# Kernel optimization log

Measured on AMD Instinct MI355X. Metric: run time of the kernel, lower is better.

The kernel has to match this reference:

```python
import jax, jax.numpy as jnp
import numpy as np

DF = 16
B, D, H, W = 2, 64, 64, 64


def _shift(a, axis, s):
    """Return a shifted so out[i] = a[i+s] along `axis`, zero-padded."""
    pad = [(0, 0)] * a.ndim
    pad[axis] = (1, 1)
    ap = jnp.pad(a, pad)
    idx = [slice(None)] * a.ndim
    idx[axis] = slice(1 + s, 1 + s + a.shape[axis])
    return ap[tuple(idx)]


def _image_grad(x, sum_axis):
    """Faithful replica of ImageGradient's (buggy) dense kernel.

    Uses only input channel 1; central difference along W; summed over the
    3 taps along `sum_axis` (1=D for pos==1, 2=H for pos==2); result is
    identical across all output channels.
    x: [B, C, D, H, W] -> [B, C, D, H, W]
    """
    s = x[:, 1]  # [B, D, H, W]
    g = 0.5 * (_shift(s, 3, 1) - _shift(s, 3, -1))  # d/dW central diff
    g3 = _shift(g, sum_axis, -1) + g + _shift(g, sum_axis, 1)
    return jnp.broadcast_to(g3[:, None], x.shape)


def _pconv(x, w, b):
    """nn.Conv3d(cin, cout, 1, padding=1): zero-pad spatial dims then 1x1x1 conv."""
    xp = jnp.pad(x, ((0, 0), (0, 0), (1, 1), (1, 1), (1, 1)))
    return jnp.einsum('bcdhw,oc->bodhw', xp, w) + b[None, :, None, None, None]


def setup_inputs() -> dict:
    key = jax.random.key(0)
    ks = jax.random.split(key, 8)
    p = jax.random.normal(ks[0], (B, DF, D, H, W), dtype=jnp.float32)
    q = jax.random.normal(ks[1], (B, DF, D, H, W), dtype=jnp.float32)
    W1 = jax.random.normal(ks[2], (DF, 6 * DF), dtype=jnp.float32) / np.sqrt(6 * DF)
    b1 = jax.random.normal(ks[3], (DF,), dtype=jnp.float32) * 0.01
    W2 = jax.random.normal(ks[4], (DF, DF), dtype=jnp.float32) / np.sqrt(DF)
    b2 = jax.random.normal(ks[5], (DF,), dtype=jnp.float32) * 0.01
    W3 = jax.random.normal(ks[6], (1, DF), dtype=jnp.float32) / np.sqrt(DF)
    b3 = jax.random.normal(ks[7], (1,), dtype=jnp.float32) * 0.01
    return {"p": p, "q": q, "W1": W1, "b1": b1, "W2": W2, "b2": b2, "W3": W3, "b3": b3}


def reference(p, q, W1, b1, W2, b2, W3, b3):
    dpx = _image_grad(p, 1)  # gradx: pos==1, sum over kd (D axis)
    dpy = _image_grad(p, 2)  # grady: pos==2, sum over kh (H axis)
    dqx = _image_grad(q, 1)
    dqy = _image_grad(q, 2)
    h = jnp.concatenate([p, dpx, dpy, q, dqx, dqy], axis=1)  # [B, 6*DF, D, H, W]
    h = jax.nn.relu(_pconv(h, W1, b1))  # [B, DF, D+2, H+2, W+2]
    h = jax.nn.relu(_pconv(h, W2, b2))  # [B, DF, D+4, H+4, W+4]
    h = jax.nn.relu(_pconv(h, W3, b3))  # [B, 1, D+6, H+6, W+6]
    return (h, p, dpx, dpy, q, dqx, dqy)
```

## Files before the change

kernel.cpp:

```cpp
#include <hip/hip_runtime.h>

#define N3   (64*64*64)
#define NO   70
#define NO3  (NO*NO*NO)
#define OH   (2*NO3)
#define SZ   (2*16*N3)

__device__ __forceinline__ float relu(float x){ return x > 0.f ? x : 0.f; }

__global__ __launch_bounds__(256) void ham_fused(
    const float* __restrict__ p, const float* __restrict__ q,
    const float* __restrict__ W1, const float* __restrict__ b1,
    const float* __restrict__ W2, const float* __restrict__ b2,
    const float* __restrict__ W3, const float* __restrict__ b3p,
    float* __restrict__ out)
{
    __shared__ float WpT[16][16];
    __shared__ float WqT[16][16];
    __shared__ float W2l[16][16];
    __shared__ float b1l[16], b2l[16], W3l[16];
    __shared__ float s1x[16], s1y[16], s2x[16], s2y[16];

    int t = threadIdx.x;
    {
        int o = t >> 4, c = t & 15;
        WpT[c][o] = W1[o*96 + c];
        WqT[c][o] = W1[o*96 + 48 + c];
        W2l[o][c] = W2[o*16 + c];
    }
    if (t < 16) {
        b1l[t] = b1[t]; b2l[t] = b2[t]; W3l[t] = W3[t];
        float ax=0.f, ay=0.f, bx=0.f, by=0.f;
        #pragma unroll
        for (int j = 0; j < 16; ++j) {
            ax += W1[t*96 + 16 + j];
            ay += W1[t*96 + 32 + j];
            bx += W1[t*96 + 64 + j];
            by += W1[t*96 + 80 + j];
        }
        s1x[t]=ax; s1y[t]=ay; s2x[t]=bx; s2y[t]=by;
    }
    __syncthreads();

    int idx = blockIdx.x * 256 + t;
    if (idx >= OH) return;

    int b = idx / NO3;
    int r = idx - b*NO3;
    int d = r / (NO*NO); r -= d*(NO*NO);
    int h = r / NO;
    int w = r - h*NO;

    float b3v = b3p[0];
    float outv;

    if ((unsigned)(d-1) >= 68u || (unsigned)(h-1) >= 68u || (unsigned)(w-1) >= 68u) {
        outv = relu(b3v);
    } else {
        float y2[16];
        if ((unsigned)(d-2) >= 66u || (unsigned)(h-2) >= 66u || (unsigned)(w-2) >= 66u) {
            #pragma unroll
            for (int o = 0; o < 16; ++o) y2[o] = relu(b2l[o]);
        } else {
            float y1[16];
            int d0 = d-3, h0 = h-3, w0 = w-3;
            bool interior = (unsigned)d0 < 64u && (unsigned)h0 < 64u && (unsigned)w0 < 64u;
            if (!interior) {
                #pragma unroll
                for (int c = 0; c < 16; ++c) y1[c] = relu(b1l[c]);
            } else {
                const float* ps = p + (b*16 + 1)*N3;
                const float* qs = q + (b*16 + 1)*N3;
                auto ld = [&](const float* s, int dd, int hh, int ww) -> float {
                    if ((unsigned)dd >= 64u || (unsigned)hh >= 64u || (unsigned)ww >= 64u)
                        return 0.f;
                    return s[dd*4096 + hh*64 + ww];
                };
                auto g = [&](const float* s, int dd, int hh, int ww) -> float {
                    return 0.5f*(ld(s, dd, hh, ww+1) - ld(s, dd, hh, ww-1));
                };
                float gcp = g(ps, d0, h0, w0);
                float dpx = g(ps, d0-1, h0, w0) + gcp + g(ps, d0+1, h0, w0);
                float dpy = g(ps, d0, h0-1, w0) + gcp + g(ps, d0, h0+1, w0);
                float gcq = g(qs, d0, h0, w0);
                float dqx = g(qs, d0-1, h0, w0) + gcq + g(qs, d0+1, h0, w0);
                float dqy = g(qs, d0, h0-1, w0) + gcq + g(qs, d0, h0+1, w0);

                #pragma unroll
                for (int o = 0; o < 16; ++o)
                    y1[o] = b1l[o] + s1x[o]*dpx + s1y[o]*dpy + s2x[o]*dqx + s2y[o]*dqy;

                int sbase = d0*4096 + h0*64 + w0;
                int ibase = b*16*N3 + sbase;

                float* outp  = out + OH;
                float* outdx = out + OH + SZ;
                float* outdy = out + OH + 2*SZ;
                float* outq  = out + OH + 3*SZ;
                float* outqx = out + OH + 4*SZ;
                float* outqy = out + OH + 5*SZ;

                #pragma unroll
                for (int c = 0; c < 16; ++c) {
                    float pc = p[ibase + c*N3];
                    float qc = q[ibase + c*N3];
                    outp[ibase + c*N3] = pc;
                    outq[ibase + c*N3] = qc;
                    #pragma unroll
                    for (int o = 0; o < 16; ++o)
                        y1[o] += WpT[c][o]*pc + WqT[c][o]*qc;
                }
                #pragma unroll
                for (int c = 0; c < 16; ++c) {
                    outdx[ibase + c*N3] = dpx;
                    outdy[ibase + c*N3] = dpy;
                    outqx[ibase + c*N3] = dqx;
                    outqy[ibase + c*N3] = dqy;
                }
                #pragma unroll
                for (int o = 0; o < 16; ++o) y1[o] = relu(y1[o]);
            }
            #pragma unroll
            for (int o = 0; o < 16; ++o) {
                float a = b2l[o];
                #pragma unroll
                for (int c = 0; c < 16; ++c) a += W2l[o][c]*y1[c];
                y2[o] = relu(a);
            }
        }
        float a = b3v;
        #pragma unroll
        for (int c = 0; c < 16; ++c) a += W3l[c]*y2[c];
        outv = relu(a);
    }
    out[idx] = outv;
}

extern "C" void kernel_launch(void* const* d_in, const int* in_sizes, int n_in,
                              void* d_out, int out_size, void* d_ws, size_t ws_size,
                              hipStream_t stream) {
    const float* p  = (const float*)d_in[0];
    const float* q  = (const float*)d_in[1];
    const float* W1 = (const float*)d_in[2];
    const float* b1 = (const float*)d_in[3];
    const float* W2 = (const float*)d_in[4];
    const float* b2 = (const float*)d_in[5];
    const float* W3 = (const float*)d_in[6];
    const float* b3 = (const float*)d_in[7];
    float* out = (float*)d_out;

    int total = OH;
    int blocks = (total + 255) / 256;
    ham_fused<<<blocks, 256, 0, stream>>>(p, q, W1, b1, W2, b2, W3, b3, out);
}
```

Measured before the change: 343.8 us.

## Split interior/border kernels and vectorize interior to 4 voxels per thread

Separates the work into an interior kernel that processes four consecutive W voxels per thread with float4 loads and nontemporal float4 stores, and a lightweight border kernel that fills the padded halo with constant values. This removes the divergent branching of the single fused kernel and cuts the number of address computations and scalar memory transactions. The cost is an extra kernel launch, higher register pressure from holding 4x16 accumulators, and a border kernel that still scans the full padded output index space.

New measurement: 380.5 us. +10.7%, slower.

```diff
diff --git a/kernel.cpp b/kernel.cpp
--- a/kernel.cpp
+++ b/kernel.cpp
@@ -2,13 +2,16 @@
 
 #define N3   (64*64*64)
 #define NO   70
+#define NO2  (NO*NO)
 #define NO3  (NO*NO*NO)
 #define OH   (2*NO3)
 #define SZ   (2*16*N3)
 
+typedef __attribute__((ext_vector_type(4))) float f4;
+
 __device__ __forceinline__ float relu(float x){ return x > 0.f ? x : 0.f; }
 
-__global__ __launch_bounds__(256) void ham_fused(
+__global__ __launch_bounds__(256) void ham_interior(
     const float* __restrict__ p, const float* __restrict__ q,
     const float* __restrict__ W1, const float* __restrict__ b1,
     const float* __restrict__ W2, const float* __restrict__ b2,
@@ -42,98 +45,154 @@
     }
     __syncthreads();
 
-    int idx = blockIdx.x * 256 + t;
-    if (idx >= OH) return;
-
-    int b = idx / NO3;
-    int r = idx - b*NO3;
-    int d = r / (NO*NO); r -= d*(NO*NO);
+    int i  = blockIdx.x * 256 + t;
+    int w4 = i & 15;  int w0 = w4 << 2;
+    int r  = i >> 4;
+    int h0 = r & 63;  r >>= 6;
+    int d0 = r & 63;  int b = r >> 6;
+
+    float b3v = b3p[0];
+
+    const float* ps = p + (b*16 + 1)*N3;
+    const float* qs = q + (b*16 + 1)*N3;
+
+    auto row6 = [&](const float* s, int dd, int hh, float rr[6]) {
+        if ((unsigned)dd >= 64u || (unsigned)hh >= 64u) {
+            #pragma unroll
+            for (int j = 0; j < 6; ++j) rr[j] = 0.f;
+            return;
+        }
+        const float* rp = s + dd*4096 + hh*64 + w0;
+        f4 v = *(const f4*)rp;
+        rr[1]=v[0]; rr[2]=v[1]; rr[3]=v[2]; rr[4]=v[3];
+        rr[0] = (w4 > 0)  ? rp[-1] : 0.f;
+        rr[5] = (w4 < 15) ? rp[4]  : 0.f;
+    };
+
+    float dpx[4], dpy[4], dqx[4], dqy[4];
+    {
+        float rc[6], ra[6], rb[6], gc[4];
+        row6(ps, d0,   h0,   rc);
+        row6(ps, d0-1, h0,   ra);
+        row6(ps, d0+1, h0,   rb);
+        #pragma unroll
+        for (int j = 0; j < 4; ++j) gc[j]  = 0.5f*(rc[j+2]-rc[j]);
+        #pragma unroll
+        for (int j = 0; j < 4; ++j) dpx[j] = 0.5f*(ra[j+2]-ra[j]) + gc[j] + 0.5f*(rb[j+2]-rb[j]);
+        row6(ps, d0, h0-1, ra);
+        row6(ps, d0, h0+1, rb);
+        #pragma unroll
+        for (int j = 0; j < 4; ++j) dpy[j] = 0.5f*(ra[j+2]-ra[j]) + gc[j] + 0.5f*(rb[j+2]-rb[j]);
+
+        row6(qs, d0,   h0,   rc);
+        row6(qs, d0-1, h0,   ra);
+        row6(qs, d0+1, h0,   rb);
+        #pragma unroll
+        for (int j = 0; j < 4; ++j) gc[j]  = 0.5f*(rc[j+2]-rc[j]);
+        #pragma unroll
+        for (int j = 0; j < 4; ++j) dqx[j] = 0.5f*(ra[j+2]-ra[j]) + gc[j] + 0.5f*(rb[j+2]-rb[j]);
+        row6(qs, d0, h0-1, ra);
+        row6(qs, d0, h0+1, rb);
+        #pragma unroll
+        for (int j = 0; j < 4; ++j) dqy[j] = 0.5f*(ra[j+2]-ra[j]) + gc[j] + 0.5f*(rb[j+2]-rb[j]);
+    }
+
+    float y1[4][16];
+    #pragma unroll
+    for (int j = 0; j < 4; ++j)
+        #pragma unroll
+        for (int o = 0; o < 16; ++o)
+            y1[j][o] = b1l[o] + s1x[o]*dpx[j] + s1y[o]*dpy[j]
+                              + s2x[o]*dqx[j] + s2y[o]*dqy[j];
+
+    int ibase = b*16*N3 + d0*4096 + h0*64 + w0;
+
+    float* outp  = out + OH;
+    float* outdx = out + OH + SZ;
+    float* outdy = out + OH + 2*SZ;
+    float* outq  = out + OH + 3*SZ;
+    float* outqx = out + OH + 4*SZ;
+    float* outqy = out + OH + 5*SZ;
+
+    #pragma unroll
+    for (int c = 0; c < 16; ++c) {
+        f4 pc = *(const f4*)(p + ibase + c*N3);
+        f4 qc = *(const f4*)(q + ibase + c*N3);
+        __builtin_nontemporal_store(pc, (f4*)(outp + ibase + c*N3));
+        __builtin_nontemporal_store(qc, (f4*)(outq + ibase + c*N3));
+        #pragma unroll
+        for (int o = 0; o < 16; ++o) {
+            float wp = WpT[c][o], wq = WqT[c][o];
+            #pragma unroll
+            for (int j = 0; j < 4; ++j)
+                y1[j][o] += wp*pc[j] + wq*qc[j];
+        }
+    }
+
+    f4 vdx, vdy, vqx, vqy;
+    #pragma unroll
+    for (int j = 0; j < 4; ++j) { vdx[j]=dpx[j]; vdy[j]=dpy[j]; vqx[j]=dqx[j]; vqy[j]=dqy[j]; }
+    #pragma unroll
+    for (int c = 0; c < 16; ++c) {
+        __builtin_nontemporal_store(vdx, (f4*)(outdx + ibase + c*N3));
+        __builtin_nontemporal_store(vdy, (f4*)(outdy + ibase + c*N3));
+        __builtin_nontemporal_store(vqx, (f4*)(outqx + ibase + c*N3));
+        __builtin_nontemporal_store(vqy, (f4*)(outqy + ibase + c*N3));
+    }
+
+    int obase = b*NO3 + (d0+3)*NO2 + (h0+3)*NO + (w0+3);
+    #pragma unroll
+    for (int j = 0; j < 4; ++j) {
+        float acc = b3v;
+        #pragma unroll
+        for (int o = 0; o < 16; ++o) {
+            float a2 = b2l[o];
+            #pragma unroll
+            for (int c = 0; c < 16; ++c) a2 += W2l[o][c]*relu(y1[j][c]);
+            acc += W3l[o]*relu(a2);
+        }
+        out[obase + j] = relu(acc);
+    }
+}
+
+__global__ __launch_bounds__(256) void ham_border(
+    const float* __restrict__ b1, const float* __restrict__ W2,
+    const float* __restrict__ b2, const float* __restrict__ W3,
+    const float* __restrict__ b3p, float* __restrict__ out)
+{
+    int i = blockIdx.x * 256 + threadIdx.x;
+    if (i >= OH) return;
+
+    int b = i / NO3;
+    int r = i - b*NO3;
+    int d = r / NO2; r -= d*NO2;
     int h = r / NO;
     int w = r - h*NO;
+    (void)b;
+
+    if ((unsigned)(d-3) < 64u && (unsigned)(h-3) < 64u && (unsigned)(w-3) < 64u) return;
 
     float b3v = b3p[0];
-    float outv;
-
+    float val;
     if ((unsigned)(d-1) >= 68u || (unsigned)(h-1) >= 68u || (unsigned)(w-1) >= 68u) {
-        outv = relu(b3v);
+        val = relu(b3v);
+    } else if ((unsigned)(d-2) >= 66u || (unsigned)(h-2) >= 66u || (unsigned)(w-2) >= 66u) {
+        float acc = b3v;
+        #pragma unroll
+        for (int o = 0; o < 16; ++o) acc += W3[o]*relu(b2[o]);
+        val = relu(acc);
     } else {
-        float y2[16];
-        if ((unsigned)(d-2) >= 66u || (unsigned)(h-2) >= 66u || (unsigned)(w-2) >= 66u) {
-            #pragma unroll
-            for (int o = 0; o < 16; ++o) y2[o] = relu(b2l[o]);
-        } else {
-            float y1[16];
-            int d0 = d-3, h0 = h-3, w0 = w-3;
-            bool interior = (unsigned)d0 < 64u && (unsigned)h0 < 64u && (unsigned)w0 < 64u;
-            if (!interior) {
-                #pragma unroll
-                for (int c = 0; c < 16; ++c) y1[c] = relu(b1l[c]);
-            } else {
-                const float* ps = p + (b*16 + 1)*N3;
-                const float* qs = q + (b*16 + 1)*N3;
-                auto ld = [&](const float* s, int dd, int hh, int ww) -> float {
-                    if ((unsigned)dd >= 64u || (unsigned)hh >= 64u || (unsigned)ww >= 64u)
-                        return 0.f;
-                    return s[dd*4096 + hh*64 + ww];
-                };
-                auto g = [&](const float* s, int dd, int hh, int ww) -> float {
-                    return 0.5f*(ld(s, dd, hh, ww+1) - ld(s, dd, hh, ww-1));
-                };
-                float gcp = g(ps, d0, h0, w0);
-                float dpx = g(ps, d0-1, h0, w0) + gcp + g(ps, d0+1, h0, w0);
-                float dpy = g(ps, d0, h0-1, w0) + gcp + g(ps, d0, h0+1, w0);
-                float gcq = g(qs, d0, h0, w0);
-                float dqx = g(qs, d0-1, h0, w0) + gcq + g(qs, d0+1, h0, w0);
-                float dqy = g(qs, d0, h0-1, w0) + gcq + g(qs, d0, h0+1, w0);
-
-                #pragma unroll
-                for (int o = 0; o < 16; ++o)
-                    y1[o] = b1l[o] + s1x[o]*dpx + s1y[o]*dpy + s2x[o]*dqx + s2y[o]*dqy;
-
-                int sbase = d0*4096 + h0*64 + w0;
-                int ibase = b*16*N3 + sbase;
-
-                float* outp  = out + OH;
-                float* outdx = out + OH + SZ;
-                float* outdy = out + OH + 2*SZ;
-                float* outq  = out + OH + 3*SZ;
-                float* outqx = out + OH + 4*SZ;
-                float* outqy = out + OH + 5*SZ;
-
-                #pragma unroll
-                for (int c = 0; c < 16; ++c) {
-                    float pc = p[ibase + c*N3];
-                    float qc = q[ibase + c*N3];
-                    outp[ibase + c*N3] = pc;
-                    outq[ibase + c*N3] = qc;
-                    #pragma unroll
-                    for (int o = 0; o < 16; ++o)
-                        y1[o] += WpT[c][o]*pc + WqT[c][o]*qc;
-                }
-                #pragma unroll
-                for (int c = 0; c < 16; ++c) {
-                    outdx[ibase + c*N3] = dpx;
-                    outdy[ibase + c*N3] = dpy;
-                    outqx[ibase + c*N3] = dqx;
-                    outqy[ibase + c*N3] = dqy;
-                }
-                #pragma unroll
-                for (int o = 0; o < 16; ++o) y1[o] = relu(y1[o]);
-            }
-            #pragma unroll
-            for (int o = 0; o < 16; ++o) {
-                float a = b2l[o];
-                #pragma unroll
-                for (int c = 0; c < 16; ++c) a += W2l[o][c]*y1[c];
-                y2[o] = relu(a);
-            }
-        }
-        float a = b3v;
-        #pragma unroll
-        for (int c = 0; c < 16; ++c) a += W3l[c]*y2[c];
-        outv = relu(a);
-    }
-    out[idx] = outv;
+        float acc = b3v;
+        #pragma unroll
+        for (int o = 0; o < 16; ++o) {
+            float a2 = b2[o];
+            #pragma unroll
+            for (int c = 0; c < 16; ++c) a2 += W2[o*16 + c]*relu(b1[c]);
+            acc += W3[o]*relu(a2);
+        }
+        val = relu(acc);
+    }
+    out[i] = val;
 }
 
 extern "C" void kernel_launch(void* const* d_in, const int* in_sizes, int n_in,
@@ -149,7 +208,6 @@
     const float* b3 = (const float*)d_in[7];
     float* out = (float*)d_out;
 
-    int total = OH;
-    int blocks = (total + 255) / 256;
-    ham_fused<<<blocks, 256, 0, stream>>>(p, q, W1, b1, W2, b2, W3, b3, out);
+    ham_interior<<<512, 256, 0, stream>>>(p, q, W1, b1, W2, b2, W3, b3, out);
+    ham_border<<<(OH + 255)/256, 256, 0, stream>>>(b1, W2, b2, W3, b3, out);
 }
```
